# Performance work log

Hardware: AMD Instinct MI355X
Metric: run time of the kernel (lower is better)

The kernel has to match this reference:

```python
import jax, jax.numpy as jnp
import numpy as np

NUM_CODES = 512
CODE_DIM = 64
COMMITMENT_COST = 0.25


def setup_inputs() -> dict:
    key = jax.random.key(0)
    k1, k2 = jax.random.split(key)
    latents = jax.random.normal(k1, (32, 64, 64, CODE_DIM), dtype=jnp.float32)
    # torch init: uniform(-1/num_codes, 1/num_codes)
    codebook = jax.random.uniform(
        k2, (NUM_CODES, CODE_DIM), dtype=jnp.float32,
        minval=-1.0 / NUM_CODES, maxval=1.0 / NUM_CODES)
    return {"latents": latents, "codebook": codebook}


def reference(latents, codebook):
    shape = latents.shape
    flat = latents.reshape(-1, CODE_DIM)  # [N, D]
    # argmin of squared distance == argmin of cdist(p=2) distance.
    x2 = jnp.sum(flat * flat, axis=-1, keepdims=True)           # [N, 1]
    c2 = jnp.sum(codebook * codebook, axis=-1)                   # [K]
    d2 = x2 - 2.0 * (flat @ codebook.T) + c2[None, :]            # [N, K]
    codes_flat = jnp.argmin(d2, axis=-1)                         # [N] int
    codes = codes_flat.reshape(shape[:-1])

    quantized = codebook[codes_flat].reshape(shape)              # gather

    commitment = jnp.mean(jnp.square(latents - jax.lax.stop_gradient(quantized)))
    codebook_loss = jnp.mean(jnp.square(quantized - jax.lax.stop_gradient(latents)))

    # straight-through estimator
    quantized_st = latents + jax.lax.stop_gradient(quantized - latents)

    # perplexity histogram
    counts = jnp.bincount(codes_flat, length=NUM_CODES).astype(jnp.float32)
    probs = counts / jnp.sum(counts)
    entropy = -jnp.sum(probs * jnp.log(probs + 1e-10))
    perplexity = jnp.exp(entropy)

    return (quantized_st, codes,
            commitment * COMMITMENT_COST, codebook_loss, perplexity)
```

## Files before the change

kernel.cpp:

```cpp
#include <hip/hip_runtime.h>
#include <math.h>

#define N_ROWS 131072
#define DIMS 64
#define K_CODES 512
#define XS_STRIDE 68

typedef __attribute__((ext_vector_type(8))) short bf16x8;
typedef __attribute__((ext_vector_type(4))) float f32x4;

union B8 { uint4 u; bf16x8 h; };

__device__ inline unsigned bpack(float a, float b) {
  unsigned ua = __float_as_uint(a), ub = __float_as_uint(b);
  ua = (ua + 0x7FFFu + ((ua >> 16) & 1u)) >> 16;
  ub = (ub + 0x7FFFu + ((ub >> 16) & 1u)) >> 16;
  return ua | (ub << 16);
}

__device__ inline float exact_dot(const float* __restrict__ xr, const float* __restrict__ cr) {
  float m = 0.f;
  #pragma unroll
  for (int d4 = 0; d4 < 16; ++d4) {
    const float4 c = *(const float4*)&cr[d4 * 4];
    const float4 x = *(const float4*)&xr[d4 * 4];
    m = fmaf(x.x, c.x, m);
    m = fmaf(x.y, c.y, m);
    m = fmaf(x.z, c.z, m);
    m = fmaf(x.w, c.w, m);
  }
  return m;
}

__global__ __launch_bounds__(256) void vq_init(const float* __restrict__ codebook,
                                               int* __restrict__ bins,
                                               float* __restrict__ c2g,
                                               float* __restrict__ cmax2p,
                                               uint4* __restrict__ cbB) {
  #pragma clang fp contract(off)
  __shared__ float smax[256];
  const int t = threadIdx.x;
  const int b = blockIdx.x;
  if (b == 0) {
    for (int k = t; k < K_CODES; k += 256) bins[k] = 0;
    float lmax = 0.f;
    for (int k = t; k < K_CODES; k += 256) {
      const float* cr = codebook + k * DIMS;
      float r[8];
      #pragma unroll
      for (int j = 0; j < 8; ++j) r[j] = cr[j] * cr[j];
      for (int i = 8; i < 64; i += 8) {
        #pragma unroll
        for (int j = 0; j < 8; ++j) r[j] += cr[i + j] * cr[i + j];
      }
      const float c2 = ((r[0] + r[1]) + (r[2] + r[3])) + ((r[4] + r[5]) + (r[6] + r[7]));
      c2g[k] = c2;
      lmax = fmaxf(lmax, c2);
    }
    smax[t] = lmax;
    __syncthreads();
    for (int s = 128; s > 0; s >>= 1) {
      if (t < s) smax[t] = fmaxf(smax[t], smax[t + s]);
      __syncthreads();
    }
    if (t == 0) *cmax2p = smax[0];
  }
  if (b < 16) {
    const int e = b * 256 + t;
    const int ct = e >> 7;
    const int q = e & 127;
    const int lane_id = q >> 1;
    const int half = q & 1;
    const int code = ct * 16 + (lane_id & 15);
    const int dbase = ((lane_id >> 4) * 8) + half * 32;
    const float* src = codebook + code * DIMS + dbase;
    const float4 a = *(const float4*)&src[0];
    const float4 c = *(const float4*)&src[4];
    uint4 u;
    u.x = bpack(a.x, a.y);
    u.y = bpack(a.z, a.w);
    u.z = bpack(c.x, c.y);
    u.w = bpack(c.z, c.w);
    cbB[e] = u;
  }
}

__global__ __launch_bounds__(256) void vq_main(const float* __restrict__ latents,
                                               const float* __restrict__ codebook,
                                               const uint4* __restrict__ cbB,
                                               const float* __restrict__ c2g,
                                               const float* __restrict__ cmax2p,
                                               float* __restrict__ out_st,
                                               float* __restrict__ out_codes,
                                               int* __restrict__ bins,
                                               double* __restrict__ loss_part) {
  #pragma clang fp contract(off)
  __shared__ __align__(16) float xs[64 * XS_STRIDE];
  __shared__ float x2s[64];
  __shared__ float c2s[K_CODES];
  __shared__ float thr[64];
  __shared__ int cand_cnt[64];
  __shared__ int cand_k[64][16];
  __shared__ int rowk[64];
  __shared__ float pvv[4][64];
  __shared__ int pkk[4][64];
  __shared__ int ovf_rows[64];
  __shared__ int ovf_cnt;
  __shared__ double wsum[4];

  const int t = threadIdx.x;
  const int lane = t & 63;
  const int w = t >> 6;
  const int row0 = blockIdx.x * 64;

  {
    const float4* src = (const float4*)(latents + (size_t)row0 * DIMS);
    #pragma unroll
    for (int p = 0; p < 4; ++p) {
      const int f = p * 256 + t;
      *(float4*)&xs[(f >> 4) * XS_STRIDE + (f & 15) * 4] = src[f];
    }
    c2s[t] = c2g[t];
    c2s[t + 256] = c2g[t + 256];
    if (t < 64) cand_cnt[t] = 0;
    if (t == 0) ovf_cnt = 0;
  }
  __syncthreads();

  if (t < 64) {
    const float* xr = xs + t * XS_STRIDE;
    float r[8];
    #pragma unroll
    for (int j = 0; j < 8; ++j) r[j] = xr[j] * xr[j];
    #pragma unroll
    for (int i = 8; i < 64; i += 8) {
      #pragma unroll
      for (int j = 0; j < 8; ++j) r[j] += xr[i + j] * xr[i + j];
    }
    x2s[t] = ((r[0] + r[1]) + (r[2] + r[3])) + ((r[4] + r[5]) + (r[6] + r[7]));
  }
  __syncthreads();

  const int m = lane & 15;
  const int kq = lane >> 4;
  bf16x8 af0, af1;
  {
    const float* xr = xs + (w * 16 + m) * XS_STRIDE + kq * 8;
    const float4 a0 = *(const float4*)&xr[0];
    const float4 a1 = *(const float4*)&xr[4];
    const float4 b0 = *(const float4*)&xr[32];
    const float4 b1 = *(const float4*)&xr[36];
    B8 pa, pb;
    pa.u.x = bpack(a0.x, a0.y); pa.u.y = bpack(a0.z, a0.w);
    pa.u.z = bpack(a1.x, a1.y); pa.u.w = bpack(a1.z, a1.w);
    pb.u.x = bpack(b0.x, b0.y); pb.u.y = bpack(b0.z, b0.w);
    pb.u.z = bpack(b1.x, b1.y); pb.u.w = bpack(b1.z, b1.w);
    af0 = pa.h;
    af1 = pb.h;
  }

  float x2r[4];
  int rowc[4];
  #pragma unroll
  for (int j = 0; j < 4; ++j) { rowc[j] = w * 16 + kq * 4 + j; x2r[j] = x2s[rowc[j]]; }
  const float cmax = sqrtf(*cmax2p) * 1.0001f;

  float mv0 = __builtin_inff(), mv1 = __builtin_inff(), mv2 = __builtin_inff(), mv3 = __builtin_inff();
  #pragma unroll 1
  for (int ct = 0; ct < 32; ++ct) {
    B8 b0, b1;
    b0.u = cbB[(ct * 64 + lane) * 2 + 0];
    b1.u = cbB[(ct * 64 + lane) * 2 + 1];
    f32x4 acc = {0.f, 0.f, 0.f, 0.f};
    acc = __builtin_amdgcn_mfma_f32_16x16x32_bf16(af0, b0.h, acc, 0, 0, 0);
    acc = __builtin_amdgcn_mfma_f32_16x16x32_bf16(af1, b1.h, acc, 0, 0, 0);
    const float c2v = c2s[ct * 16 + m];
    const float s0 = (x2r[0] - 2.0f * acc[0]) + c2v;
    const float s1 = (x2r[1] - 2.0f * acc[1]) + c2v;
    const float s2 = (x2r[2] - 2.0f * acc[2]) + c2v;
    const float s3 = (x2r[3] - 2.0f * acc[3]) + c2v;
    mv0 = fminf(mv0, s0); mv1 = fminf(mv1, s1);
    mv2 = fminf(mv2, s2); mv3 = fminf(mv3, s3);
  }
  #pragma unroll
  for (int off = 1; off < 16; off <<= 1) {
    mv0 = fminf(mv0, __shfl_xor(mv0, off));
    mv1 = fminf(mv1, __shfl_xor(mv1, off));
    mv2 = fminf(mv2, __shfl_xor(mv2, off));
    mv3 = fminf(mv3, __shfl_xor(mv3, off));
  }
  if (m == 0) {
    thr[rowc[0]] = mv0 + (sqrtf(x2r[0]) * cmax * 0.0427f + 1e-3f);
    thr[rowc[1]] = mv1 + (sqrtf(x2r[1]) * cmax * 0.0427f + 1e-3f);
    thr[rowc[2]] = mv2 + (sqrtf(x2r[2]) * cmax * 0.0427f + 1e-3f);
    thr[rowc[3]] = mv3 + (sqrtf(x2r[3]) * cmax * 0.0427f + 1e-3f);
  }
  __syncthreads();

  float thrr[4];
  #pragma unroll
  for (int j = 0; j < 4; ++j) thrr[j] = thr[rowc[j]];
  #pragma unroll 1
  for (int ct = 0; ct < 32; ++ct) {
    B8 b0, b1;
    b0.u = cbB[(ct * 64 + lane) * 2 + 0];
    b1.u = cbB[(ct * 64 + lane) * 2 + 1];
    f32x4 acc = {0.f, 0.f, 0.f, 0.f};
    acc = __builtin_amdgcn_mfma_f32_16x16x32_bf16(af0, b0.h, acc, 0, 0, 0);
    acc = __builtin_amdgcn_mfma_f32_16x16x32_bf16(af1, b1.h, acc, 0, 0, 0);
    const float c2v = c2s[ct * 16 + m];
    const int k = ct * 16 + m;
    #pragma unroll
    for (int j = 0; j < 4; ++j) {
      const float s = (x2r[j] - 2.0f * acc[j]) + c2v;
      if (s <= thrr[j]) {
        const int pos = atomicAdd(&cand_cnt[rowc[j]], 1);
        if (pos < 16) cand_k[rowc[j]][pos] = k;
      }
    }
  }
  __syncthreads();

  {
    const int rr = t & 63;
    const int ph = t >> 6;
    const int cnt = cand_cnt[rr];
    float bv = __builtin_inff();
    int bk = 0x7fffffff;
    if (cnt <= 16) {
      const float* xr = xs + rr * XS_STRIDE;
      const float x2e = x2s[rr];
      for (int c = ph; c < cnt; c += 4) {
        const int k = cand_k[rr][c];
        const float M = exact_dot(xr, codebook + k * DIMS);
        const float s = (x2e - 2.0f * M) + c2s[k];
        if (s < bv || (s == bv && k < bk)) { bv = s; bk = k; }
      }
    } else if (ph == 0) {
      const int p = atomicAdd(&ovf_cnt, 1);
      ovf_rows[p] = rr;
    }
    pvv[ph][rr] = bv;
    pkk[ph][rr] = bk;
  }
  __syncthreads();
  if (t < 64) {
    float bv = pvv[0][t];
    int bk = pkk[0][t];
    #pragma unroll
    for (int ph = 1; ph < 4; ++ph) {
      const float v = pvv[ph][t];
      const int k = pkk[ph][t];
      if (v < bv || (v == bv && k < bk)) { bv = v; bk = k; }
    }
    rowk[t] = bk;
  }
  __syncthreads();

  if (w == 0) {
    const int no = ovf_cnt;
    for (int o = 0; o < no; ++o) {
      const int rr = ovf_rows[o];
      const float* xr = xs + rr * XS_STRIDE;
      const float x2e = x2s[rr];
      float bv = __builtin_inff();
      int bk = 0x7fffffff;
      for (int k = lane; k < K_CODES; k += 64) {
        const float M = exact_dot(xr, codebook + k * DIMS);
        const float s = (x2e - 2.0f * M) + c2s[k];
        if (s < bv || (s == bv && k < bk)) { bv = s; bk = k; }
      }
      #pragma unroll
      for (int off = 1; off < 64; off <<= 1) {
        const float ov = __shfl_xor(bv, off);
        const int oi = __shfl_xor(bk, off);
        if (ov < bv || (ov == bv && oi < bk)) { bv = ov; bk = oi; }
      }
      if (lane == 0) rowk[rr] = bk;
    }
  }
  __syncthreads();

  if (t < 64) {
    const int k = rowk[t];
    out_codes[row0 + t] = (float)k;
    atomicAdd(&bins[k], 1);
  }
  double dacc = 0.0;
  {
    float4* dst = (float4*)out_st + (size_t)row0 * 16;
    #pragma unroll
    for (int p = 0; p < 4; ++p) {
      const int f = p * 256 + t;
      const int r = f >> 4;
      const int d4 = f & 15;
      const int k = rowk[r];
      const float4 q = *(const float4*)&codebook[k * DIMS + d4 * 4];
      const float4 l = *(const float4*)&xs[r * XS_STRIDE + d4 * 4];
      float4 o;
      o.x = l.x + (q.x - l.x);
      o.y = l.y + (q.y - l.y);
      o.z = l.z + (q.z - l.z);
      o.w = l.w + (q.w - l.w);
      dst[f] = o;
      const float dx = l.x - q.x, dy = l.y - q.y, dz = l.z - q.z, dw = l.w - q.w;
      dacc += (double)dx * (double)dx;
      dacc += (double)dy * (double)dy;
      dacc += (double)dz * (double)dz;
      dacc += (double)dw * (double)dw;
    }
  }
  #pragma unroll
  for (int off = 32; off > 0; off >>= 1) dacc += __shfl_down(dacc, off);
  if (lane == 0) wsum[w] = dacc;
  __syncthreads();
  if (t == 0) loss_part[blockIdx.x] = (wsum[0] + wsum[1]) + (wsum[2] + wsum[3]);
}

__global__ __launch_bounds__(512) void vq_finalize(const int* __restrict__ bins,
                                                   const double* __restrict__ loss_part,
                                                   float* __restrict__ out3) {
  __shared__ double red[512];
  __shared__ double redl[512];
  const int t = threadIdx.x;
  const double p = (double)bins[t] / 131072.0;
  red[t] = -p * log(p + 1e-10);
  redl[t] = (loss_part[t] + loss_part[t + 512]) + (loss_part[t + 1024] + loss_part[t + 1536]);
  __syncthreads();
  for (int s = 256; s > 0; s >>= 1) {
    if (t < s) { red[t] += red[t + s]; redl[t] += redl[t + s]; }
    __syncthreads();
  }
  if (t == 0) {
    const double mean = redl[0] / 8388608.0;
    out3[0] = (float)(0.25 * mean);
    out3[1] = (float)mean;
    out3[2] = (float)exp(red[0]);
  }
}

extern "C" void kernel_launch(void* const* d_in, const int* in_sizes, int n_in,
                              void* d_out, int out_size, void* d_ws, size_t ws_size,
                              hipStream_t stream) {
  const float* latents = (const float*)d_in[0];
  const float* codebook = (const float*)d_in[1];

  float* out = (float*)d_out;
  float* out_st = out;
  float* out_codes = out + (size_t)N_ROWS * DIMS;
  float* out3 = out_codes + N_ROWS;

  char* ws = (char*)d_ws;
  double* loss_part = (double*)ws;
  int* bins = (int*)(ws + 16384);
  float* c2g = (float*)(ws + 18432);
  float* cmax2 = (float*)(ws + 20480);
  uint4* cbB = (uint4*)(ws + 21504);

  hipLaunchKernelGGL(vq_init, dim3(16), dim3(256), 0, stream,
                     codebook, bins, c2g, cmax2, cbB);
  hipLaunchKernelGGL(vq_main, dim3(2048), dim3(256), 0, stream,
                     latents, codebook, cbB, c2g, cmax2, out_st, out_codes, bins, loss_part);
  hipLaunchKernelGGL(vq_finalize, dim3(1), dim3(512), 0, stream,
                     bins, loss_part, out3);
}
```

Measured before the change: 169.9 us.

## Split codebook across waves and reuse each codebook tile over all row tiles

Each wave previously handled 16 rows against all 32 codebook tiles. Now each wave handles all 64 rows (4 A-fragments held in registers) against its own 8-tile slice of the codebook, and per-wave minima are merged through shared memory before the threshold is computed. This cuts global/L2 codebook fragment loads per block by 4x. It also adds register prefetch of the next codebook tile and sets a launch_bounds occupancy hint. In exchange it uses more registers for fragments and accumulators and adds an extra barrier and shared-memory reduction.

```diff
diff --git a/kernel.cpp b/kernel.cpp
--- a/kernel.cpp
+++ b/kernel.cpp
@@ -85,20 +85,21 @@
   }
 }
 
-__global__ __launch_bounds__(256) void vq_main(const float* __restrict__ latents,
-                                               const float* __restrict__ codebook,
-                                               const uint4* __restrict__ cbB,
-                                               const float* __restrict__ c2g,
-                                               const float* __restrict__ cmax2p,
-                                               float* __restrict__ out_st,
-                                               float* __restrict__ out_codes,
-                                               int* __restrict__ bins,
-                                               double* __restrict__ loss_part) {
+__global__ __launch_bounds__(256, 4) void vq_main(const float* __restrict__ latents,
+                                                  const float* __restrict__ codebook,
+                                                  const uint4* __restrict__ cbB,
+                                                  const float* __restrict__ c2g,
+                                                  const float* __restrict__ cmax2p,
+                                                  float* __restrict__ out_st,
+                                                  float* __restrict__ out_codes,
+                                                  int* __restrict__ bins,
+                                                  double* __restrict__ loss_part) {
   #pragma clang fp contract(off)
   __shared__ __align__(16) float xs[64 * XS_STRIDE];
   __shared__ float x2s[64];
   __shared__ float c2s[K_CODES];
   __shared__ float thr[64];
+  __shared__ float pmin[4][64];
   __shared__ int cand_cnt[64];
   __shared__ int cand_k[64][16];
   __shared__ int rowk[64];
@@ -111,6 +112,8 @@
   const int t = threadIdx.x;
   const int lane = t & 63;
   const int w = t >> 6;
+  const int m = lane & 15;
+  const int kq = lane >> 4;
   const int row0 = blockIdx.x * 64;
 
   {
@@ -141,11 +144,10 @@
   }
   __syncthreads();
 
-  const int m = lane & 15;
-  const int kq = lane >> 4;
-  bf16x8 af0, af1;
-  {
-    const float* xr = xs + (w * 16 + m) * XS_STRIDE + kq * 8;
+  bf16x8 af0[4], af1[4];
+  #pragma unroll
+  for (int T = 0; T < 4; ++T) {
+    const float* xr = xs + (T * 16 + m) * XS_STRIDE + kq * 8;
     const float4 a0 = *(const float4*)&xr[0];
     const float4 a1 = *(const float4*)&xr[4];
     const float4 b0 = *(const float4*)&xr[32];
@@ -155,69 +157,105 @@
     pa.u.z = bpack(a1.x, a1.y); pa.u.w = bpack(a1.z, a1.w);
     pb.u.x = bpack(b0.x, b0.y); pb.u.y = bpack(b0.z, b0.w);
     pb.u.z = bpack(b1.x, b1.y); pb.u.w = bpack(b1.z, b1.w);
-    af0 = pa.h;
-    af1 = pb.h;
-  }
-
-  float x2r[4];
-  int rowc[4];
-  #pragma unroll
-  for (int j = 0; j < 4; ++j) { rowc[j] = w * 16 + kq * 4 + j; x2r[j] = x2s[rowc[j]]; }
+    af0[T] = pa.h;
+    af1[T] = pb.h;
+  }
+
+  float x2r[4][4];
+  #pragma unroll
+  for (int T = 0; T < 4; ++T)
+    #pragma unroll
+    for (int j = 0; j < 4; ++j) x2r[T][j] = x2s[T * 16 + kq * 4 + j];
   const float cmax = sqrtf(*cmax2p) * 1.0001f;
-
-  float mv0 = __builtin_inff(), mv1 = __builtin_inff(), mv2 = __builtin_inff(), mv3 = __builtin_inff();
+  const int ct0 = w * 8;
+
+  float mv[4][4];
+  #pragma unroll
+  for (int T = 0; T < 4; ++T)
+    #pragma unroll
+    for (int j = 0; j < 4; ++j) mv[T][j] = __builtin_inff();
+
+  B8 cb0, cb1, nb0, nb1;
+  cb0.u = cbB[ct0 * 128 + lane * 2 + 0];
+  cb1.u = cbB[ct0 * 128 + lane * 2 + 1];
   #pragma unroll 1
-  for (int ct = 0; ct < 32; ++ct) {
-    B8 b0, b1;
-    b0.u = cbB[(ct * 64 + lane) * 2 + 0];
-    b1.u = cbB[(ct * 64 + lane) * 2 + 1];
-    f32x4 acc = {0.f, 0.f, 0.f, 0.f};
-    acc = __builtin_amdgcn_mfma_f32_16x16x32_bf16(af0, b0.h, acc, 0, 0, 0);
-    acc = __builtin_amdgcn_mfma_f32_16x16x32_bf16(af1, b1.h, acc, 0, 0, 0);
+  for (int q = 0; q < 8; ++q) {
+    const int ct = ct0 + q;
+    if (q < 7) {
+      nb0.u = cbB[(ct + 1) * 128 + lane * 2 + 0];
+      nb1.u = cbB[(ct + 1) * 128 + lane * 2 + 1];
+    }
     const float c2v = c2s[ct * 16 + m];
-    const float s0 = (x2r[0] - 2.0f * acc[0]) + c2v;
-    const float s1 = (x2r[1] - 2.0f * acc[1]) + c2v;
-    const float s2 = (x2r[2] - 2.0f * acc[2]) + c2v;
-    const float s3 = (x2r[3] - 2.0f * acc[3]) + c2v;
-    mv0 = fminf(mv0, s0); mv1 = fminf(mv1, s1);
-    mv2 = fminf(mv2, s2); mv3 = fminf(mv3, s3);
-  }
-  #pragma unroll
-  for (int off = 1; off < 16; off <<= 1) {
-    mv0 = fminf(mv0, __shfl_xor(mv0, off));
-    mv1 = fminf(mv1, __shfl_xor(mv1, off));
-    mv2 = fminf(mv2, __shfl_xor(mv2, off));
-    mv3 = fminf(mv3, __shfl_xor(mv3, off));
-  }
+    #pragma unroll
+    for (int T = 0; T < 4; ++T) {
+      f32x4 acc = {0.f, 0.f, 0.f, 0.f};
+      acc = __builtin_amdgcn_mfma_f32_16x16x32_bf16(af0[T], cb0.h, acc, 0, 0, 0);
+      acc = __builtin_amdgcn_mfma_f32_16x16x32_bf16(af1[T], cb1.h, acc, 0, 0, 0);
+      #pragma unroll
+      for (int j = 0; j < 4; ++j) {
+        const float s = (x2r[T][j] - 2.0f * acc[j]) + c2v;
+        mv[T][j] = fminf(mv[T][j], s);
+      }
+    }
+    cb0 = nb0;
+    cb1 = nb1;
+  }
+  #pragma unroll
+  for (int T = 0; T < 4; ++T)
+    #pragma unroll
+    for (int j = 0; j < 4; ++j) {
+      float v = mv[T][j];
+      #pragma unroll
+      for (int off = 1; off < 16; off <<= 1) v = fminf(v, __shfl_xor(v, off));
+      mv[T][j] = v;
+    }
   if (m == 0) {
-    thr[rowc[0]] = mv0 + (sqrtf(x2r[0]) * cmax * 0.0427f + 1e-3f);
-    thr[rowc[1]] = mv1 + (sqrtf(x2r[1]) * cmax * 0.0427f + 1e-3f);
-    thr[rowc[2]] = mv2 + (sqrtf(x2r[2]) * cmax * 0.0427f + 1e-3f);
-    thr[rowc[3]] = mv3 + (sqrtf(x2r[3]) * cmax * 0.0427f + 1e-3f);
-  }
-  __syncthreads();
-
-  float thrr[4];
-  #pragma unroll
-  for (int j = 0; j < 4; ++j) thrr[j] = thr[rowc[j]];
+    #pragma unroll
+    for (int T = 0; T < 4; ++T)
+      #pragma unroll
+      for (int j = 0; j < 4; ++j) pmin[w][T * 16 + kq * 4 + j] = mv[T][j];
+  }
+  __syncthreads();
+  if (t < 64) {
+    const float gmin = fminf(fminf(pmin[0][t], pmin[1][t]), fminf(pmin[2][t], pmin[3][t]));
+    thr[t] = gmin + (sqrtf(x2s[t]) * cmax * 0.0427f + 1e-3f);
+  }
+  __syncthreads();
+
+  float thrr[4][4];
+  #pragma unroll
+  for (int T = 0; T < 4; ++T)
+    #pragma unroll
+    for (int j = 0; j < 4; ++j) thrr[T][j] = thr[T * 16 + kq * 4 + j];
+
+  cb0.u = cbB[ct0 * 128 + lane * 2 + 0];
+  cb1.u = cbB[ct0 * 128 + lane * 2 + 1];
   #pragma unroll 1
-  for (int ct = 0; ct < 32; ++ct) {
-    B8 b0, b1;
-    b0.u = cbB[(ct * 64 + lane) * 2 + 0];
-    b1.u = cbB[(ct * 64 + lane) * 2 + 1];
-    f32x4 acc = {0.f, 0.f, 0.f, 0.f};
-    acc = __builtin_amdgcn_mfma_f32_16x16x32_bf16(af0, b0.h, acc, 0, 0, 0);
-    acc = __builtin_amdgcn_mfma_f32_16x16x32_bf16(af1, b1.h, acc, 0, 0, 0);
+  for (int q = 0; q < 8; ++q) {
+    const int ct = ct0 + q;
+    if (q < 7) {
+      nb0.u = cbB[(ct + 1) * 128 + lane * 2 + 0];
+      nb1.u = cbB[(ct + 1) * 128 + lane * 2 + 1];
+    }
     const float c2v = c2s[ct * 16 + m];
     const int k = ct * 16 + m;
     #pragma unroll
-    for (int j = 0; j < 4; ++j) {
-      const float s = (x2r[j] - 2.0f * acc[j]) + c2v;
-      if (s <= thrr[j]) {
-        const int pos = atomicAdd(&cand_cnt[rowc[j]], 1);
-        if (pos < 16) cand_k[rowc[j]][pos] = k;
-      }
-    }
+    for (int T = 0; T < 4; ++T) {
+      f32x4 acc = {0.f, 0.f, 0.f, 0.f};
+      acc = __builtin_amdgcn_mfma_f32_16x16x32_bf16(af0[T], cb0.h, acc, 0, 0, 0);
+      acc = __builtin_amdgcn_mfma_f32_16x16x32_bf16(af1[T], cb1.h, acc, 0, 0, 0);
+      #pragma unroll
+      for (int j = 0; j < 4; ++j) {
+        const float s = (x2r[T][j] - 2.0f * acc[j]) + c2v;
+        if (s <= thrr[T][j]) {
+          const int rr = T * 16 + kq * 4 + j;
+          const int pos = atomicAdd(&cand_cnt[rr], 1);
+          if (pos < 16) cand_k[rr][pos] = k;
+        }
+      }
+    }
+    cb0 = nb0;
+    cb1 = nb1;
   }
   __syncthreads();
 
```

After: 152.6 us. 10.2% less time.
